# Kernel optimization log

Hardware: AMD Instinct MI355X
Metric: run time of the kernel (lower is better)

Reference implementation:

```python
import jax, jax.numpy as jnp
import numpy as np

N, M, BS = 32, 64, 512
ALPHA, BETA = 1.0, 1.0


def setup_inputs() -> dict:
    key = jax.random.key(0)
    k1, k2, k3, k4 = jax.random.split(key, 4)
    q = jax.random.normal(k1, (BS, N), jnp.float32)
    b = jax.random.normal(k2, (BS, M), jnp.float32)
    A0 = jax.random.normal(k3, (N, N), jnp.float32)
    P = A0 @ A0.T / N + jnp.eye(N, dtype=jnp.float32)  # SPD cost matrix
    H = jax.random.normal(k4, (M, N), jnp.float32) / jnp.sqrt(jnp.float32(N))
    return {"q": q, "b": b, "P": P, "H": H, "iters": 1000}


def reference(q, b, P, H, iters):
    m = H.shape[0]
    # Pinv-applied quantities via solve (matches torch.linalg.solve / pinv usage)
    Pinv_q = jnp.linalg.solve(P, q.T).T                 # (bs, n)
    D = H @ jnp.linalg.solve(P, H.T)                    # (m, m) = H P^-1 H^T
    # dummy preconditioner: scaled identity keeping the operator nonexpansive
    lam_max = jnp.linalg.eigvalsh(D)[-1]
    tD = (BETA / lam_max) * jnp.eye(m, dtype=q.dtype)   # (m, m)
    mu = ((H @ Pinv_q.T).T - b) @ tD.T                  # (bs, m)
    tDD = tD @ D
    I = jnp.eye(m, dtype=q.dtype)
    A = jnp.block([[tDD, tD],
                   [-2.0 * ALPHA * tDD + I, I - 2.0 * ALPHA * tD]])  # (2m, 2m)
    B = jnp.concatenate([mu, -2.0 * ALPHA * mu], axis=1)             # (bs, 2m)
    Hinv = jnp.linalg.pinv(H)                            # (n, m)
    X0 = jnp.zeros((q.shape[0], 2 * m), q.dtype)

    def step(X, _):
        X = X @ A.T + B
        X = X.at[:, m:].set(jax.nn.relu(X[:, m:]))       # in-place ReLU on dual half
        return X, X

    _, ys = jax.lax.scan(step, X0, None, length=iters)   # (iters, bs, 2m)
    Xs = jnp.concatenate([X0[None], ys], axis=0).transpose(1, 0, 2)  # (bs, iters+1, 2m)
    # primal_sols[k] = Hinv @ (X_k[m:] - b)
    primal_sols = jnp.einsum('nm,bkm->bkn', Hinv, Xs[:, :, m:] - b[:, None, :])
    return Xs, primal_sols
```

## Files before the change

### kernel.cpp

```cpp
#include <hip/hip_runtime.h>
#include <math.h>

#define BATCH 512
#define ITERS 1000

#define OFF_S    0
#define OFF_SD   16
#define OFF_PHT  (16 + 4096)
#define OFF_HINV (16 + 4096 + 2048)

__device__ __forceinline__ float rdlane(float v, int l) {
  return __int_as_float(__builtin_amdgcn_readlane(__float_as_int(v), l));
}

#define GJ32_REG(g)                                            \
  _Pragma("unroll")                                            \
  for (int k = 0; k < 32; ++k) {                               \
    float inv = 1.0f / rdlane(g[k], k);                        \
    g[k] *= inv;                                               \
    _Pragma("unroll")                                          \
    for (int i = 0; i < 32; ++i) {                             \
      if (i == k) continue;                                    \
      float f = rdlane(g[i], k);                               \
      g[i] = fmaf(-f, g[k], g[i]);                             \
    }                                                          \
  }

__global__ __launch_bounds__(64) void setup_kernel(const float* __restrict__ P,
                                                   const float* __restrict__ H,
                                                   float* __restrict__ ws) {
  __shared__ float Hl[64][36];
  const int lane = threadIdx.x;

  float hreg[32];
  {
    const float4* hp = (const float4*)(H + lane * 32);
    #pragma unroll
    for (int j4 = 0; j4 < 8; ++j4) {
      float4 t = hp[j4];
      hreg[4*j4+0] = t.x; hreg[4*j4+1] = t.y; hreg[4*j4+2] = t.z; hreg[4*j4+3] = t.w;
    }
  }

  if (blockIdx.x == 0) {
    float g[32];
    #pragma unroll
    for (int r = 0; r < 32; ++r) {
      float pv = P[r*32 + (lane & 31)];
      g[r] = (lane < 32) ? pv : (((lane - 32) == r) ? 1.0f : 0.0f);
    }
    GJ32_REG(g)

    float pht[32];
    #pragma unroll
    for (int r = 0; r < 32; ++r) {
      float a0 = 0.f, a1 = 0.f;
      #pragma unroll
      for (int j = 0; j < 32; j += 2) {
        a0 = fmaf(rdlane(g[r], 32 + j),     hreg[j],     a0);
        a1 = fmaf(rdlane(g[r], 32 + j + 1), hreg[j + 1], a1);
      }
      pht[r] = a0 + a1;
      ws[OFF_PHT + r*64 + lane] = pht[r];
    }

    float dcol[64];
    #pragma unroll
    for (int r = 0; r < 64; ++r) {
      float a0 = 0.f, a1 = 0.f;
      #pragma unroll
      for (int j = 0; j < 32; j += 2) {
        a0 = fmaf(rdlane(hreg[j],     r), pht[j],     a0);
        a1 = fmaf(rdlane(hreg[j + 1], r), pht[j + 1], a1);
      }
      dcol[r] = a0 + a1;
    }

    float ecol[64];
    #pragma unroll
    for (int r = 0; r < 64; ++r) {
      float a0 = 0.f, a1 = 0.f;
      #pragma unroll
      for (int c = 0; c < 64; c += 2) {
        a0 = fmaf(rdlane(dcol[r], c),     dcol[c],     a0);
        a1 = fmaf(rdlane(dcol[r], c + 1), dcol[c + 1], a1);
      }
      ecol[r] = a0 + a1;
    }

    float v = 1.0f + 0.017f * (float)lane;
    #pragma unroll 1
    for (int t = 0; t < 112; ++t) {
      float a0 = 0.f, a1 = 0.f, a2 = 0.f, a3 = 0.f;
      #pragma unroll
      for (int c = 0; c < 64; c += 4) {
        a0 = fmaf(ecol[c+0], rdlane(v, c+0), a0);
        a1 = fmaf(ecol[c+1], rdlane(v, c+1), a1);
        a2 = fmaf(ecol[c+2], rdlane(v, c+2), a2);
        a3 = fmaf(ecol[c+3], rdlane(v, c+3), a3);
      }
      v = (a0 + a1) + (a2 + a3);
      if ((t & 7) == 7) {
        float n2 = v * v;
        #pragma unroll
        for (int m = 1; m < 64; m <<= 1) n2 += __shfl_xor(n2, m);
        v *= 1.0f / sqrtf(n2);
      }
    }
    {
      float a0 = 0.f, a1 = 0.f, a2 = 0.f, a3 = 0.f;
      #pragma unroll
      for (int c = 0; c < 64; c += 4) {
        a0 = fmaf(dcol[c+0], rdlane(v, c+0), a0);
        a1 = fmaf(dcol[c+1], rdlane(v, c+1), a1);
        a2 = fmaf(dcol[c+2], rdlane(v, c+2), a2);
        a3 = fmaf(dcol[c+3], rdlane(v, c+3), a3);
      }
      float w = (a0 + a1) + (a2 + a3);
      float num = w * v, den = v * v;
      #pragma unroll
      for (int m = 1; m < 64; m <<= 1) {
        num += __shfl_xor(num, m);
        den += __shfl_xor(den, m);
      }
      float s = den / num;
      if (lane == 0) ws[OFF_S] = s;
      #pragma unroll
      for (int r = 0; r < 64; ++r) ws[OFF_SD + r*64 + lane] = s * dcol[r];
    }
  } else {
    #pragma unroll
    for (int j = 0; j < 32; ++j) Hl[lane][j] = hreg[j];
    __syncthreads();
    float htc[64];
    #pragma unroll
    for (int m = 0; m < 64; ++m) htc[m] = Hl[m][lane & 31];

    float gB[32];
    #pragma unroll
    for (int r = 0; r < 32; ++r) {
      float a0 = 0.f, a1 = 0.f;
      #pragma unroll
      for (int m = 0; m < 64; m += 2) {
        a0 = fmaf(rdlane(hreg[r], m),     htc[m],     a0);
        a1 = fmaf(rdlane(hreg[r], m + 1), htc[m + 1], a1);
      }
      float hth = a0 + a1;
      gB[r] = (lane < 32) ? hth : (((lane - 32) == r) ? 1.0f : 0.0f);
    }
    GJ32_REG(gB)
    #pragma unroll
    for (int r = 0; r < 32; ++r) {
      float a0 = 0.f, a1 = 0.f;
      #pragma unroll
      for (int j = 0; j < 32; j += 2) {
        a0 = fmaf(rdlane(gB[r], 32 + j),     hreg[j],     a0);
        a1 = fmaf(rdlane(gB[r], 32 + j + 1), hreg[j + 1], a1);
      }
      ws[OFF_HINV + r*64 + lane] = a0 + a1;
    }
  }
}

__global__ __launch_bounds__(64) void iter_kernel(const float* __restrict__ q,
                                                  const float* __restrict__ bmat,
                                                  const float* __restrict__ ws,
                                                  float* __restrict__ Xs) {
  const int row = blockIdx.x, lane = threadIdx.x;

  float sdr[64];
  {
    const float4* sp = (const float4*)(ws + OFF_SD + lane * 64);
    #pragma unroll
    for (int j4 = 0; j4 < 16; ++j4) {
      float4 t = sp[j4];
      sdr[4*j4+0] = t.x; sdr[4*j4+1] = t.y; sdr[4*j4+2] = t.z; sdr[4*j4+3] = t.w;
    }
  }
  const float s = ws[OFF_S];
  float acc = 0.f;
  {
    const float* qrow = q + row * 32;
    #pragma unroll
    for (int j = 0; j < 32; ++j) acc = fmaf(qrow[j], ws[OFF_PHT + j*64 + lane], acc);
  }
  const float mu = s * (acc - bmat[row * 64 + lane]);

  float x1 = 0.f, x2 = 0.f;
  float* Xp = Xs + (size_t)row * (ITERS + 1) * 128;
  Xp[lane] = 0.f;
  Xp[64 + lane] = 0.f;

  #pragma unroll 1
  for (int k = 1; k <= ITERS; ++k) {
    float a0 = 0.f, a1 = 0.f, a2 = 0.f, a3 = 0.f;
    #pragma unroll
    for (int j = 0; j < 64; j += 4) {
      a0 = fmaf(sdr[j+0], rdlane(x1, j+0), a0);
      a1 = fmaf(sdr[j+1], rdlane(x1, j+1), a1);
      a2 = fmaf(sdr[j+2], rdlane(x1, j+2), a2);
      a3 = fmaf(sdr[j+3], rdlane(x1, j+3), a3);
    }
    float x1n = ((a0 + a1) + (a2 + a3)) + fmaf(s, x2, mu);
    float x2n = fmaxf(x1 + x2 - 2.0f * x1n, 0.f);
    Xp += 128;
    Xp[lane] = x1n;
    Xp[64 + lane] = x2n;
    x1 = x1n; x2 = x2n;
  }
}

__global__ __launch_bounds__(512) void primal_kernel(const float* __restrict__ bmat,
                                                     const float* __restrict__ ws,
                                                     const float* __restrict__ Xs,
                                                     float* __restrict__ out2) {
  const int row = blockIdx.x;
  const int tid = threadIdx.x;
  const int wv = tid >> 6, lane = tid & 63;
  const int i = lane & 31, h = lane >> 5;
  __shared__ __align__(16) float tbuf[8][64];

  float hv[32];
  {
    const float4* hp = (const float4*)(ws + OFF_HINV + i * 64 + h * 32);
    #pragma unroll
    for (int j4 = 0; j4 < 8; ++j4) {
      float4 t = hp[j4];
      hv[4*j4+0] = t.x; hv[4*j4+1] = t.y; hv[4*j4+2] = t.z; hv[4*j4+3] = t.w;
    }
  }
  const float bl = bmat[row * 64 + lane];
  const float* Xb = Xs + (size_t)row * (ITERS + 1) * 128 + 64;
  float* ob = out2 + (size_t)row * (ITERS + 1) * 32;

  float tA = Xb[(size_t)wv * 128 + lane] - bl;
  float tB = (wv + 8 <= ITERS) ? Xb[(size_t)(wv + 8) * 128 + lane] - bl : 0.f;

  #pragma unroll 1
  for (int k = wv; k <= ITERS; k += 8) {
    const int kn = k + 16;
    float tC = (kn <= ITERS) ? Xb[(size_t)kn * 128 + lane] - bl : 0.f;
    tbuf[wv][lane] = tA;
    __builtin_amdgcn_wave_barrier();
    float a0 = 0.f, a1 = 0.f, a2 = 0.f, a3 = 0.f;
    const float4* tp = (const float4*)&tbuf[wv][h * 32];
    #pragma unroll
    for (int j4 = 0; j4 < 8; ++j4) {
      float4 t = tp[j4];
      a0 = fmaf(hv[4*j4+0], t.x, a0);
      a1 = fmaf(hv[4*j4+1], t.y, a1);
      a2 = fmaf(hv[4*j4+2], t.z, a2);
      a3 = fmaf(hv[4*j4+3], t.w, a3);
    }
    float p = (a0 + a1) + (a2 + a3);
    p += __shfl_xor(p, 32);
    if (h == 0) ob[(size_t)k * 32 + i] = p;
    __builtin_amdgcn_wave_barrier();
    tA = tB; tB = tC;
  }
}

extern "C" void kernel_launch(void* const* d_in, const int* in_sizes, int n_in,
                              void* d_out, int out_size, void* d_ws, size_t ws_size,
                              hipStream_t stream) {
  (void)in_sizes; (void)n_in; (void)out_size; (void)ws_size;
  const float* q = (const float*)d_in[0];
  const float* b = (const float*)d_in[1];
  const float* P = (const float*)d_in[2];
  const float* H = (const float*)d_in[3];
  float* ws = (float*)d_ws;
  float* Xs = (float*)d_out;
  float* out2 = Xs + (size_t)BATCH * (ITERS + 1) * 128;

  setup_kernel<<<2, 64, 0, stream>>>(P, H, ws);
  iter_kernel<<<BATCH, 64, 0, stream>>>(q, b, ws, Xs);
  primal_kernel<<<BATCH, 512, 0, stream>>>(b, ws, Xs, out2);
}
```

Baseline: 685.1 us.

## Fuse setup, iteration and primal projection into one kernel per batch row

Merges the three kernels into one. Each block redundantly recomputes the setup quantities (P inverse, H pseudo-inverse, the power-iteration eigenvalue and the scaled D) and then runs the recurrence. The primal projection for step k-1 is computed inside step k from a double-buffered LDS copy of the dual half, so the primal kernel no longer has to read Xs back from global memory and the extra launches and workspace traffic disappear. The cost is that every one of the 512 blocks repeats the serial setup work, about two 32x32 Gauss-Jordan eliminations plus 112 power iterations, before its loop can start.

```diff
diff --git a/kernel.cpp b/kernel.cpp
--- a/kernel.cpp
+++ b/kernel.cpp
@@ -4,13 +4,18 @@
 #define BATCH 512
 #define ITERS 1000
 
-#define OFF_S    0
-#define OFF_SD   16
-#define OFF_PHT  (16 + 4096)
-#define OFF_HINV (16 + 4096 + 2048)
+typedef float f32x2 __attribute__((ext_vector_type(2)));
+typedef float f32x4 __attribute__((ext_vector_type(4)));
 
 __device__ __forceinline__ float rdlane(float v, int l) {
   return __int_as_float(__builtin_amdgcn_readlane(__float_as_int(v), l));
+}
+__device__ __forceinline__ f32x2 fma2(f32x2 a, f32x2 b, f32x2 c) {
+#if __has_builtin(__builtin_elementwise_fma)
+  return __builtin_elementwise_fma(a, b, c);
+#else
+  f32x2 r; r.x = fmaf(a.x, b.x, c.x); r.y = fmaf(a.y, b.y, c.y); return r;
+#endif
 }
 
 #define GJ32_REG(g)                                            \
@@ -19,39 +24,88 @@
     float inv = 1.0f / rdlane(g[k], k);                        \
     g[k] *= inv;                                               \
     _Pragma("unroll")                                          \
-    for (int i = 0; i < 32; ++i) {                             \
-      if (i == k) continue;                                    \
-      float f = rdlane(g[i], k);                               \
-      g[i] = fmaf(-f, g[k], g[i]);                             \
+    for (int ii = 0; ii < 32; ++ii) {                          \
+      if (ii == k) continue;                                   \
+      float f = rdlane(g[ii], k);                              \
+      g[ii] = fmaf(-f, g[k], g[ii]);                           \
     }                                                          \
   }
 
-__global__ __launch_bounds__(64) void setup_kernel(const float* __restrict__ P,
-                                                   const float* __restrict__ H,
-                                                   float* __restrict__ ws) {
-  __shared__ float Hl[64][36];
-  const int lane = threadIdx.x;
+__global__ __launch_bounds__(64, 1)
+void fused_kernel(const float* __restrict__ q,
+                  const float* __restrict__ bmat,
+                  const float* __restrict__ P,
+                  const float* __restrict__ H,
+                  float* __restrict__ Xs,
+                  float* __restrict__ out2) {
+  __shared__ __align__(16) float lds[2112 + 128];
+  float* Hlp = lds;
+  float* HTp = lds;
+  float* xb  = lds + 2112;
+
+  const int row = blockIdx.x, lane = threadIdx.x;
+  const int i = lane & 31, h = lane >> 5;
+
+  const float bl = bmat[row * 64 + lane];
 
   float hreg[32];
   {
-    const float4* hp = (const float4*)(H + lane * 32);
+    const f32x4* hp = (const f32x4*)(H + lane * 32);
     #pragma unroll
     for (int j4 = 0; j4 < 8; ++j4) {
-      float4 t = hp[j4];
+      f32x4 t = hp[j4];
       hreg[4*j4+0] = t.x; hreg[4*j4+1] = t.y; hreg[4*j4+2] = t.z; hreg[4*j4+3] = t.w;
     }
-  }
-
-  if (blockIdx.x == 0) {
+    #pragma unroll
+    for (int j = 0; j < 32; ++j) Hlp[lane * 33 + j] = hreg[j];
+  }
+  __syncthreads();
+
+  f32x2 hv2[16];
+  {
+    float htc[64];
+    #pragma unroll
+    for (int m = 0; m < 64; ++m) htc[m] = Hlp[m * 33 + i];
+
+    float gB[32];
+    #pragma unroll
+    for (int r = 0; r < 32; ++r) {
+      float a0 = 0.f, a1 = 0.f;
+      #pragma unroll
+      for (int m = 0; m < 64; m += 2) {
+        a0 = fmaf(rdlane(hreg[r], m),     htc[m],     a0);
+        a1 = fmaf(rdlane(hreg[r], m + 1), htc[m + 1], a1);
+      }
+      float hth = a0 + a1;
+      gB[r] = (lane < 32) ? hth : (((lane - 32) == r) ? 1.0f : 0.0f);
+    }
+    GJ32_REG(gB)
+    __syncthreads();
+    #pragma unroll
+    for (int r = 0; r < 32; ++r) {
+      float a0 = 0.f, a1 = 0.f;
+      #pragma unroll
+      for (int c = 0; c < 32; c += 2) {
+        a0 = fmaf(rdlane(gB[r], 32 + c),     hreg[c],     a0);
+        a1 = fmaf(rdlane(gB[r], 32 + c + 1), hreg[c + 1], a1);
+      }
+      HTp[r * 66 + lane] = a0 + a1;
+    }
+    __syncthreads();
+    #pragma unroll
+    for (int t = 0; t < 16; ++t)
+      hv2[t] = *(const f32x2*)&HTp[i * 66 + 32 * h + 2 * t];
+  }
+
+  float pht[32], dcol[64], acc;
+  {
     float g[32];
     #pragma unroll
     for (int r = 0; r < 32; ++r) {
-      float pv = P[r*32 + (lane & 31)];
+      float pv = P[r * 32 + i];
       g[r] = (lane < 32) ? pv : (((lane - 32) == r) ? 1.0f : 0.0f);
     }
     GJ32_REG(g)
-
-    float pht[32];
     #pragma unroll
     for (int r = 0; r < 32; ++r) {
       float a0 = 0.f, a1 = 0.f;
@@ -61,21 +115,30 @@
         a1 = fmaf(rdlane(g[r], 32 + j + 1), hreg[j + 1], a1);
       }
       pht[r] = a0 + a1;
-      ws[OFF_PHT + r*64 + lane] = pht[r];
-    }
-
-    float dcol[64];
-    #pragma unroll
-    for (int r = 0; r < 64; ++r) {
-      float a0 = 0.f, a1 = 0.f;
-      #pragma unroll
-      for (int j = 0; j < 32; j += 2) {
-        a0 = fmaf(rdlane(hreg[j],     r), pht[j],     a0);
-        a1 = fmaf(rdlane(hreg[j + 1], r), pht[j + 1], a1);
-      }
-      dcol[r] = a0 + a1;
-    }
-
+    }
+  }
+  {
+    const float* qp = q + row * 32;
+    float a0 = 0.f, a1 = 0.f;
+    #pragma unroll
+    for (int r = 0; r < 32; r += 2) {
+      a0 = fmaf(qp[r],     pht[r],     a0);
+      a1 = fmaf(qp[r + 1], pht[r + 1], a1);
+    }
+    acc = a0 + a1;
+  }
+  #pragma unroll
+  for (int r = 0; r < 64; ++r) {
+    float a0 = 0.f, a1 = 0.f;
+    #pragma unroll
+    for (int j = 0; j < 32; j += 2) {
+      a0 = fmaf(rdlane(hreg[j],     r), pht[j],     a0);
+      a1 = fmaf(rdlane(hreg[j + 1], r), pht[j + 1], a1);
+    }
+    dcol[r] = a0 + a1;
+  }
+  float s;
+  {
     float ecol[64];
     #pragma unroll
     for (int r = 0; r < 64; ++r) {
@@ -87,7 +150,6 @@
       }
       ecol[r] = a0 + a1;
     }
-
     float v = 1.0f + 0.017f * (float)lane;
     #pragma unroll 1
     for (int t = 0; t < 112; ++t) {
@@ -107,172 +169,97 @@
         v *= 1.0f / sqrtf(n2);
       }
     }
-    {
-      float a0 = 0.f, a1 = 0.f, a2 = 0.f, a3 = 0.f;
-      #pragma unroll
-      for (int c = 0; c < 64; c += 4) {
-        a0 = fmaf(dcol[c+0], rdlane(v, c+0), a0);
-        a1 = fmaf(dcol[c+1], rdlane(v, c+1), a1);
-        a2 = fmaf(dcol[c+2], rdlane(v, c+2), a2);
-        a3 = fmaf(dcol[c+3], rdlane(v, c+3), a3);
-      }
-      float w = (a0 + a1) + (a2 + a3);
-      float num = w * v, den = v * v;
-      #pragma unroll
-      for (int m = 1; m < 64; m <<= 1) {
-        num += __shfl_xor(num, m);
-        den += __shfl_xor(den, m);
-      }
-      float s = den / num;
-      if (lane == 0) ws[OFF_S] = s;
-      #pragma unroll
-      for (int r = 0; r < 64; ++r) ws[OFF_SD + r*64 + lane] = s * dcol[r];
-    }
-  } else {
-    #pragma unroll
-    for (int j = 0; j < 32; ++j) Hl[lane][j] = hreg[j];
-    __syncthreads();
-    float htc[64];
-    #pragma unroll
-    for (int m = 0; m < 64; ++m) htc[m] = Hl[m][lane & 31];
-
-    float gB[32];
-    #pragma unroll
-    for (int r = 0; r < 32; ++r) {
-      float a0 = 0.f, a1 = 0.f;
-      #pragma unroll
-      for (int m = 0; m < 64; m += 2) {
-        a0 = fmaf(rdlane(hreg[r], m),     htc[m],     a0);
-        a1 = fmaf(rdlane(hreg[r], m + 1), htc[m + 1], a1);
-      }
-      float hth = a0 + a1;
-      gB[r] = (lane < 32) ? hth : (((lane - 32) == r) ? 1.0f : 0.0f);
-    }
-    GJ32_REG(gB)
-    #pragma unroll
-    for (int r = 0; r < 32; ++r) {
-      float a0 = 0.f, a1 = 0.f;
-      #pragma unroll
-      for (int j = 0; j < 32; j += 2) {
-        a0 = fmaf(rdlane(gB[r], 32 + j),     hreg[j],     a0);
-        a1 = fmaf(rdlane(gB[r], 32 + j + 1), hreg[j + 1], a1);
-      }
-      ws[OFF_HINV + r*64 + lane] = a0 + a1;
-    }
-  }
-}
-
-__global__ __launch_bounds__(64) void iter_kernel(const float* __restrict__ q,
-                                                  const float* __restrict__ bmat,
-                                                  const float* __restrict__ ws,
-                                                  float* __restrict__ Xs) {
-  const int row = blockIdx.x, lane = threadIdx.x;
-
-  float sdr[64];
-  {
-    const float4* sp = (const float4*)(ws + OFF_SD + lane * 64);
-    #pragma unroll
-    for (int j4 = 0; j4 < 16; ++j4) {
-      float4 t = sp[j4];
-      sdr[4*j4+0] = t.x; sdr[4*j4+1] = t.y; sdr[4*j4+2] = t.z; sdr[4*j4+3] = t.w;
-    }
-  }
-  const float s = ws[OFF_S];
-  float acc = 0.f;
-  {
-    const float* qrow = q + row * 32;
-    #pragma unroll
-    for (int j = 0; j < 32; ++j) acc = fmaf(qrow[j], ws[OFF_PHT + j*64 + lane], acc);
-  }
-  const float mu = s * (acc - bmat[row * 64 + lane]);
-
-  float x1 = 0.f, x2 = 0.f;
+    float a0 = 0.f, a1 = 0.f, a2 = 0.f, a3 = 0.f;
+    #pragma unroll
+    for (int c = 0; c < 64; c += 4) {
+      a0 = fmaf(dcol[c+0], rdlane(v, c+0), a0);
+      a1 = fmaf(dcol[c+1], rdlane(v, c+1), a1);
+      a2 = fmaf(dcol[c+2], rdlane(v, c+2), a2);
+      a3 = fmaf(dcol[c+3], rdlane(v, c+3), a3);
+    }
+    float w = (a0 + a1) + (a2 + a3);
+    float num = w * v, den = v * v;
+    #pragma unroll
+    for (int m = 1; m < 64; m <<= 1) {
+      num += __shfl_xor(num, m);
+      den += __shfl_xor(den, m);
+    }
+    s = den / num;
+  }
+  const float mu = s * (acc - bl);
+  #pragma unroll
+  for (int r = 0; r < 64; ++r) dcol[r] *= s;
+
   float* Xp = Xs + (size_t)row * (ITERS + 1) * 128;
+  float* ob = out2 + (size_t)row * (ITERS + 1) * 32;
   Xp[lane] = 0.f;
   Xp[64 + lane] = 0.f;
-
+  xb[lane] = -bl;
+
+  float x1 = 0.f, x2 = 0.f;
   #pragma unroll 1
   for (int k = 1; k <= ITERS; ++k) {
+    const f32x4* tp = (const f32x4*)(xb + ((k - 1) & 1) * 64 + h * 32);
+    f32x4 t0 = tp[0], t1 = tp[1], t2 = tp[2], t3 = tp[3];
+    f32x4 t4 = tp[4], t5 = tp[5], t6 = tp[6], t7 = tp[7];
+
     float a0 = 0.f, a1 = 0.f, a2 = 0.f, a3 = 0.f;
     #pragma unroll
     for (int j = 0; j < 64; j += 4) {
-      a0 = fmaf(sdr[j+0], rdlane(x1, j+0), a0);
-      a1 = fmaf(sdr[j+1], rdlane(x1, j+1), a1);
-      a2 = fmaf(sdr[j+2], rdlane(x1, j+2), a2);
-      a3 = fmaf(sdr[j+3], rdlane(x1, j+3), a3);
+      a0 = fmaf(dcol[j+0], rdlane(x1, j+0), a0);
+      a1 = fmaf(dcol[j+1], rdlane(x1, j+1), a1);
+      a2 = fmaf(dcol[j+2], rdlane(x1, j+2), a2);
+      a3 = fmaf(dcol[j+3], rdlane(x1, j+3), a3);
     }
     float x1n = ((a0 + a1) + (a2 + a3)) + fmaf(s, x2, mu);
-    float x2n = fmaxf(x1 + x2 - 2.0f * x1n, 0.f);
+    float x2n = fmaxf(fmaf(-2.0f, x1n, x1 + x2), 0.f);
     Xp += 128;
     Xp[lane] = x1n;
     Xp[64 + lane] = x2n;
+    xb[(k & 1) * 64 + lane] = x2n - bl;
+
+    f32x2 pa; pa.x = 0.f; pa.y = 0.f;
+    f32x2 pb = pa;
+    pa = fma2(hv2[0],  t0.xy, pa);  pb = fma2(hv2[1],  t0.zw, pb);
+    pa = fma2(hv2[2],  t1.xy, pa);  pb = fma2(hv2[3],  t1.zw, pb);
+    pa = fma2(hv2[4],  t2.xy, pa);  pb = fma2(hv2[5],  t2.zw, pb);
+    pa = fma2(hv2[6],  t3.xy, pa);  pb = fma2(hv2[7],  t3.zw, pb);
+    pa = fma2(hv2[8],  t4.xy, pa);  pb = fma2(hv2[9],  t4.zw, pb);
+    pa = fma2(hv2[10], t5.xy, pa);  pb = fma2(hv2[11], t5.zw, pb);
+    pa = fma2(hv2[12], t6.xy, pa);  pb = fma2(hv2[13], t6.zw, pb);
+    pa = fma2(hv2[14], t7.xy, pa);  pb = fma2(hv2[15], t7.zw, pb);
+    float p = (pa.x + pa.y) + (pb.x + pb.y);
+    p += __shfl_xor(p, 32);
+    if (h == 0) ob[(size_t)(k - 1) * 32 + i] = p;
+
     x1 = x1n; x2 = x2n;
   }
-}
-
-__global__ __launch_bounds__(512) void primal_kernel(const float* __restrict__ bmat,
-                                                     const float* __restrict__ ws,
-                                                     const float* __restrict__ Xs,
-                                                     float* __restrict__ out2) {
-  const int row = blockIdx.x;
-  const int tid = threadIdx.x;
-  const int wv = tid >> 6, lane = tid & 63;
-  const int i = lane & 31, h = lane >> 5;
-  __shared__ __align__(16) float tbuf[8][64];
-
-  float hv[32];
-  {
-    const float4* hp = (const float4*)(ws + OFF_HINV + i * 64 + h * 32);
-    #pragma unroll
-    for (int j4 = 0; j4 < 8; ++j4) {
-      float4 t = hp[j4];
-      hv[4*j4+0] = t.x; hv[4*j4+1] = t.y; hv[4*j4+2] = t.z; hv[4*j4+3] = t.w;
-    }
-  }
-  const float bl = bmat[row * 64 + lane];
-  const float* Xb = Xs + (size_t)row * (ITERS + 1) * 128 + 64;
-  float* ob = out2 + (size_t)row * (ITERS + 1) * 32;
-
-  float tA = Xb[(size_t)wv * 128 + lane] - bl;
-  float tB = (wv + 8 <= ITERS) ? Xb[(size_t)(wv + 8) * 128 + lane] - bl : 0.f;
-
-  #pragma unroll 1
-  for (int k = wv; k <= ITERS; k += 8) {
-    const int kn = k + 16;
-    float tC = (kn <= ITERS) ? Xb[(size_t)kn * 128 + lane] - bl : 0.f;
-    tbuf[wv][lane] = tA;
-    __builtin_amdgcn_wave_barrier();
-    float a0 = 0.f, a1 = 0.f, a2 = 0.f, a3 = 0.f;
-    const float4* tp = (const float4*)&tbuf[wv][h * 32];
-    #pragma unroll
-    for (int j4 = 0; j4 < 8; ++j4) {
-      float4 t = tp[j4];
-      a0 = fmaf(hv[4*j4+0], t.x, a0);
-      a1 = fmaf(hv[4*j4+1], t.y, a1);
-      a2 = fmaf(hv[4*j4+2], t.z, a2);
-      a3 = fmaf(hv[4*j4+3], t.w, a3);
-    }
-    float p = (a0 + a1) + (a2 + a3);
+  {
+    const f32x4* tp = (const f32x4*)(xb + (ITERS & 1) * 64 + h * 32);
+    f32x2 pa; pa.x = 0.f; pa.y = 0.f;
+    f32x2 pb = pa;
+    #pragma unroll
+    for (int r4 = 0; r4 < 8; ++r4) {
+      f32x4 t = tp[r4];
+      pa = fma2(hv2[2*r4],     t.xy, pa);
+      pb = fma2(hv2[2*r4 + 1], t.zw, pb);
+    }
+    float p = (pa.x + pa.y) + (pb.x + pb.y);
     p += __shfl_xor(p, 32);
-    if (h == 0) ob[(size_t)k * 32 + i] = p;
-    __builtin_amdgcn_wave_barrier();
-    tA = tB; tB = tC;
+    if (h == 0) ob[(size_t)ITERS * 32 + i] = p;
   }
 }
 
 extern "C" void kernel_launch(void* const* d_in, const int* in_sizes, int n_in,
                               void* d_out, int out_size, void* d_ws, size_t ws_size,
                               hipStream_t stream) {
-  (void)in_sizes; (void)n_in; (void)out_size; (void)ws_size;
+  (void)in_sizes; (void)n_in; (void)out_size; (void)d_ws; (void)ws_size;
   const float* q = (const float*)d_in[0];
   const float* b = (const float*)d_in[1];
   const float* P = (const float*)d_in[2];
   const float* H = (const float*)d_in[3];
-  float* ws = (float*)d_ws;
   float* Xs = (float*)d_out;
   float* out2 = Xs + (size_t)BATCH * (ITERS + 1) * 128;
 
-  setup_kernel<<<2, 64, 0, stream>>>(P, H, ws);
-  iter_kernel<<<BATCH, 64, 0, stream>>>(q, b, ws, Xs);
-  primal_kernel<<<BATCH, 512, 0, stream>>>(b, ws, Xs, out2);
-}
+  fused_kernel<<<BATCH, 64, 0, stream>>>(q, b, P, H, Xs, out2);
+}
```

Result: slower. 739.5 us (+7.9%).

## Recompute P-inverse, D and spectral scale redundantly per block inside iter kernel

Applied to the files above, without the earlier changes.

The serial setup work (Gauss-Jordan inverse of P, P^-1 H^T, D, and the 112-step power iteration for lambda_max) moves out of a single-block setup kernel into every iter_kernel block. Each block recomputes it redundantly so the iteration no longer waits on a serial setup launch and reads no workspace. The pseudo-inverse of H stays in its own small kernel. The cost is 512 copies of the setup arithmetic, with higher register pressure in iter_kernel before the main loop.

```diff
diff --git a/kernel.cpp b/kernel.cpp
--- a/kernel.cpp
+++ b/kernel.cpp
@@ -4,13 +4,18 @@
 #define BATCH 512
 #define ITERS 1000
 
-#define OFF_S    0
-#define OFF_SD   16
-#define OFF_PHT  (16 + 4096)
-#define OFF_HINV (16 + 4096 + 2048)
+typedef float f32x2 __attribute__((ext_vector_type(2)));
+typedef float f32x4 __attribute__((ext_vector_type(4)));
 
 __device__ __forceinline__ float rdlane(float v, int l) {
   return __int_as_float(__builtin_amdgcn_readlane(__float_as_int(v), l));
+}
+__device__ __forceinline__ f32x2 fma2(f32x2 a, f32x2 b, f32x2 c) {
+#if __has_builtin(__builtin_elementwise_fma)
+  return __builtin_elementwise_fma(a, b, c);
+#else
+  f32x2 r; r.x = fmaf(a.x, b.x, c.x); r.y = fmaf(a.y, b.y, c.y); return r;
+#endif
 }
 
 #define GJ32_REG(g)                                            \
@@ -19,52 +24,108 @@
     float inv = 1.0f / rdlane(g[k], k);                        \
     g[k] *= inv;                                               \
     _Pragma("unroll")                                          \
-    for (int i = 0; i < 32; ++i) {                             \
-      if (i == k) continue;                                    \
-      float f = rdlane(g[i], k);                               \
-      g[i] = fmaf(-f, g[k], g[i]);                             \
+    for (int ii = 0; ii < 32; ++ii) {                          \
+      if (ii == k) continue;                                   \
+      float f = rdlane(g[ii], k);                              \
+      g[ii] = fmaf(-f, g[k], g[ii]);                           \
     }                                                          \
   }
 
-__global__ __launch_bounds__(64) void setup_kernel(const float* __restrict__ P,
-                                                   const float* __restrict__ H,
-                                                   float* __restrict__ ws) {
-  __shared__ float Hl[64][36];
+__global__ __launch_bounds__(64) void hinv_kernel(const float* __restrict__ H,
+                                                  float* __restrict__ ws) {
+  __shared__ float hstage[64 * 34];
   const int lane = threadIdx.x;
-
+  const int l = lane & 31;
   float hreg[32];
   {
-    const float4* hp = (const float4*)(H + lane * 32);
-    #pragma unroll
-    for (int j4 = 0; j4 < 8; ++j4) {
-      float4 t = hp[j4];
+    const f32x4* hp = (const f32x4*)(H + lane * 32);
+    #pragma unroll
+    for (int j4 = 0; j4 < 8; ++j4) {
+      f32x4 t = hp[j4];
       hreg[4*j4+0] = t.x; hreg[4*j4+1] = t.y; hreg[4*j4+2] = t.z; hreg[4*j4+3] = t.w;
     }
   }
-
-  if (blockIdx.x == 0) {
-    float g[32];
-    #pragma unroll
-    for (int r = 0; r < 32; ++r) {
-      float pv = P[r*32 + (lane & 31)];
-      g[r] = (lane < 32) ? pv : (((lane - 32) == r) ? 1.0f : 0.0f);
-    }
-    GJ32_REG(g)
-
-    float pht[32];
-    #pragma unroll
-    for (int r = 0; r < 32; ++r) {
+  #pragma unroll
+  for (int j = 0; j < 32; ++j) hstage[lane * 34 + j] = hreg[j];
+  float htc[64];
+  #pragma unroll
+  for (int m = 0; m < 64; ++m) htc[m] = hstage[m * 34 + l];
+  float gB[32];
+  #pragma unroll
+  for (int r = 0; r < 32; ++r) {
+    float a0 = 0.f, a1 = 0.f;
+    #pragma unroll
+    for (int m = 0; m < 64; m += 2) {
+      a0 = fmaf(rdlane(hreg[r], m),     htc[m],     a0);
+      a1 = fmaf(rdlane(hreg[r], m + 1), htc[m + 1], a1);
+    }
+    float hth = a0 + a1;
+    gB[r] = (lane < 32) ? hth : (((lane - 32) == r) ? 1.0f : 0.0f);
+  }
+  GJ32_REG(gB)
+  #pragma unroll
+  for (int r = 0; r < 32; ++r) {
+    float a0 = 0.f, a1 = 0.f;
+    #pragma unroll
+    for (int c = 0; c < 32; c += 2) {
+      a0 = fmaf(rdlane(gB[r], 32 + c),     hreg[c],     a0);
+      a1 = fmaf(rdlane(gB[r], 32 + c + 1), hreg[c + 1], a1);
+    }
+    ws[r * 64 + lane] = a0 + a1;
+  }
+}
+
+__global__ __launch_bounds__(64) void iter_kernel(const float* __restrict__ q,
+                                                  const float* __restrict__ bmat,
+                                                  const float* __restrict__ P,
+                                                  const float* __restrict__ H,
+                                                  float* __restrict__ Xs) {
+  const int row = blockIdx.x, lane = threadIdx.x;
+  const int i = lane & 31;
+
+  float hreg[32];
+  {
+    const f32x4* hp = (const f32x4*)(H + lane * 32);
+    #pragma unroll
+    for (int j4 = 0; j4 < 8; ++j4) {
+      f32x4 t = hp[j4];
+      hreg[4*j4+0] = t.x; hreg[4*j4+1] = t.y; hreg[4*j4+2] = t.z; hreg[4*j4+3] = t.w;
+    }
+  }
+  const float bl = bmat[(size_t)row * 64 + lane];
+
+  float dcol[64], s, mu;
+  {
+    float pht[32], acc;
+    {
+      float g[32];
+      #pragma unroll
+      for (int r = 0; r < 32; ++r) {
+        float pv = P[r * 32 + i];
+        g[r] = (lane < 32) ? pv : (((lane - 32) == r) ? 1.0f : 0.0f);
+      }
+      GJ32_REG(g)
+      #pragma unroll
+      for (int r = 0; r < 32; ++r) {
+        float a0 = 0.f, a1 = 0.f;
+        #pragma unroll
+        for (int j = 0; j < 32; j += 2) {
+          a0 = fmaf(rdlane(g[r], 32 + j),     hreg[j],     a0);
+          a1 = fmaf(rdlane(g[r], 32 + j + 1), hreg[j + 1], a1);
+        }
+        pht[r] = a0 + a1;
+      }
+    }
+    {
+      const float* qp = q + (size_t)row * 32;
       float a0 = 0.f, a1 = 0.f;
       #pragma unroll
-      for (int j = 0; j < 32; j += 2) {
-        a0 = fmaf(rdlane(g[r], 32 + j),     hreg[j],     a0);
-        a1 = fmaf(rdlane(g[r], 32 + j + 1), hreg[j + 1], a1);
-      }
-      pht[r] = a0 + a1;
-      ws[OFF_PHT + r*64 + lane] = pht[r];
-    }
-
-    float dcol[64];
+      for (int r = 0; r < 32; r += 2) {
+        a0 = fmaf(qp[r],     pht[r],     a0);
+        a1 = fmaf(qp[r + 1], pht[r + 1], a1);
+      }
+      acc = a0 + a1;
+    }
     #pragma unroll
     for (int r = 0; r < 64; ++r) {
       float a0 = 0.f, a1 = 0.f;
@@ -75,39 +136,37 @@
       }
       dcol[r] = a0 + a1;
     }
-
-    float ecol[64];
-    #pragma unroll
-    for (int r = 0; r < 64; ++r) {
-      float a0 = 0.f, a1 = 0.f;
-      #pragma unroll
-      for (int c = 0; c < 64; c += 2) {
-        a0 = fmaf(rdlane(dcol[r], c),     dcol[c],     a0);
-        a1 = fmaf(rdlane(dcol[r], c + 1), dcol[c + 1], a1);
-      }
-      ecol[r] = a0 + a1;
-    }
-
-    float v = 1.0f + 0.017f * (float)lane;
-    #pragma unroll 1
-    for (int t = 0; t < 112; ++t) {
-      float a0 = 0.f, a1 = 0.f, a2 = 0.f, a3 = 0.f;
-      #pragma unroll
-      for (int c = 0; c < 64; c += 4) {
-        a0 = fmaf(ecol[c+0], rdlane(v, c+0), a0);
-        a1 = fmaf(ecol[c+1], rdlane(v, c+1), a1);
-        a2 = fmaf(ecol[c+2], rdlane(v, c+2), a2);
-        a3 = fmaf(ecol[c+3], rdlane(v, c+3), a3);
-      }
-      v = (a0 + a1) + (a2 + a3);
-      if ((t & 7) == 7) {
-        float n2 = v * v;
+    {
+      float ecol[64];
+      #pragma unroll
+      for (int r = 0; r < 64; ++r) {
+        float a0 = 0.f, a1 = 0.f;
         #pragma unroll
-        for (int m = 1; m < 64; m <<= 1) n2 += __shfl_xor(n2, m);
-        v *= 1.0f / sqrtf(n2);
-      }
-    }
-    {
+        for (int c = 0; c < 64; c += 2) {
+          a0 = fmaf(rdlane(dcol[r], c),     dcol[c],     a0);
+          a1 = fmaf(rdlane(dcol[r], c + 1), dcol[c + 1], a1);
+        }
+        ecol[r] = a0 + a1;
+      }
+      float v = 1.0f + 0.017f * (float)lane;
+      #pragma unroll 1
+      for (int t = 0; t < 112; ++t) {
+        float a0 = 0.f, a1 = 0.f, a2 = 0.f, a3 = 0.f;
+        #pragma unroll
+        for (int c = 0; c < 64; c += 4) {
+          a0 = fmaf(ecol[c+0], rdlane(v, c+0), a0);
+          a1 = fmaf(ecol[c+1], rdlane(v, c+1), a1);
+          a2 = fmaf(ecol[c+2], rdlane(v, c+2), a2);
+          a3 = fmaf(ecol[c+3], rdlane(v, c+3), a3);
+        }
+        v = (a0 + a1) + (a2 + a3);
+        if ((t & 7) == 7) {
+          float n2 = v * v;
+          #pragma unroll
+          for (int m = 1; m < 64; m <<= 1) n2 += __shfl_xor(n2, m);
+          v *= 1.0f / sqrtf(n2);
+        }
+      }
       float a0 = 0.f, a1 = 0.f, a2 = 0.f, a3 = 0.f;
       #pragma unroll
       for (int c = 0; c < 64; c += 4) {
@@ -123,68 +182,12 @@
         num += __shfl_xor(num, m);
         den += __shfl_xor(den, m);
       }
-      float s = den / num;
-      if (lane == 0) ws[OFF_S] = s;
-      #pragma unroll
-      for (int r = 0; r < 64; ++r) ws[OFF_SD + r*64 + lane] = s * dcol[r];
-    }
-  } else {
-    #pragma unroll
-    for (int j = 0; j < 32; ++j) Hl[lane][j] = hreg[j];
-    __syncthreads();
-    float htc[64];
-    #pragma unroll
-    for (int m = 0; m < 64; ++m) htc[m] = Hl[m][lane & 31];
-
-    float gB[32];
-    #pragma unroll
-    for (int r = 0; r < 32; ++r) {
-      float a0 = 0.f, a1 = 0.f;
-      #pragma unroll
-      for (int m = 0; m < 64; m += 2) {
-        a0 = fmaf(rdlane(hreg[r], m),     htc[m],     a0);
-        a1 = fmaf(rdlane(hreg[r], m + 1), htc[m + 1], a1);
-      }
-      float hth = a0 + a1;
-      gB[r] = (lane < 32) ? hth : (((lane - 32) == r) ? 1.0f : 0.0f);
-    }
-    GJ32_REG(gB)
-    #pragma unroll
-    for (int r = 0; r < 32; ++r) {
-      float a0 = 0.f, a1 = 0.f;
-      #pragma unroll
-      for (int j = 0; j < 32; j += 2) {
-        a0 = fmaf(rdlane(gB[r], 32 + j),     hreg[j],     a0);
-        a1 = fmaf(rdlane(gB[r], 32 + j + 1), hreg[j + 1], a1);
-      }
-      ws[OFF_HINV + r*64 + lane] = a0 + a1;
-    }
-  }
-}
-
-__global__ __launch_bounds__(64) void iter_kernel(const float* __restrict__ q,
-                                                  const float* __restrict__ bmat,
-                                                  const float* __restrict__ ws,
-                                                  float* __restrict__ Xs) {
-  const int row = blockIdx.x, lane = threadIdx.x;
-
-  float sdr[64];
-  {
-    const float4* sp = (const float4*)(ws + OFF_SD + lane * 64);
-    #pragma unroll
-    for (int j4 = 0; j4 < 16; ++j4) {
-      float4 t = sp[j4];
-      sdr[4*j4+0] = t.x; sdr[4*j4+1] = t.y; sdr[4*j4+2] = t.z; sdr[4*j4+3] = t.w;
-    }
-  }
-  const float s = ws[OFF_S];
-  float acc = 0.f;
-  {
-    const float* qrow = q + row * 32;
-    #pragma unroll
-    for (int j = 0; j < 32; ++j) acc = fmaf(qrow[j], ws[OFF_PHT + j*64 + lane], acc);
-  }
-  const float mu = s * (acc - bmat[row * 64 + lane]);
+      s = den / num;
+    }
+    mu = s * (acc - bl);
+    #pragma unroll
+    for (int r = 0; r < 64; ++r) dcol[r] *= s;
+  }
 
   float x1 = 0.f, x2 = 0.f;
   float* Xp = Xs + (size_t)row * (ITERS + 1) * 128;
@@ -196,13 +199,13 @@
     float a0 = 0.f, a1 = 0.f, a2 = 0.f, a3 = 0.f;
     #pragma unroll
     for (int j = 0; j < 64; j += 4) {
-      a0 = fmaf(sdr[j+0], rdlane(x1, j+0), a0);
-      a1 = fmaf(sdr[j+1], rdlane(x1, j+1), a1);
-      a2 = fmaf(sdr[j+2], rdlane(x1, j+2), a2);
-      a3 = fmaf(sdr[j+3], rdlane(x1, j+3), a3);
+      a0 = fmaf(dcol[j+0], rdlane(x1, j+0), a0);
+      a1 = fmaf(dcol[j+1], rdlane(x1, j+1), a1);
+      a2 = fmaf(dcol[j+2], rdlane(x1, j+2), a2);
+      a3 = fmaf(dcol[j+3], rdlane(x1, j+3), a3);
     }
     float x1n = ((a0 + a1) + (a2 + a3)) + fmaf(s, x2, mu);
-    float x2n = fmaxf(x1 + x2 - 2.0f * x1n, 0.f);
+    float x2n = fmaxf(fmaf(-2.0f, x1n, x1 + x2), 0.f);
     Xp += 128;
     Xp[lane] = x1n;
     Xp[64 + lane] = x2n;
@@ -222,14 +225,14 @@
 
   float hv[32];
   {
-    const float4* hp = (const float4*)(ws + OFF_HINV + i * 64 + h * 32);
-    #pragma unroll
-    for (int j4 = 0; j4 < 8; ++j4) {
-      float4 t = hp[j4];
+    const f32x4* hp = (const f32x4*)(ws + i * 64 + h * 32);
+    #pragma unroll
+    for (int j4 = 0; j4 < 8; ++j4) {
+      f32x4 t = hp[j4];
       hv[4*j4+0] = t.x; hv[4*j4+1] = t.y; hv[4*j4+2] = t.z; hv[4*j4+3] = t.w;
     }
   }
-  const float bl = bmat[row * 64 + lane];
+  const float bl = bmat[(size_t)row * 64 + lane];
   const float* Xb = Xs + (size_t)row * (ITERS + 1) * 128 + 64;
   float* ob = out2 + (size_t)row * (ITERS + 1) * 32;
 
@@ -243,10 +246,10 @@
     tbuf[wv][lane] = tA;
     __builtin_amdgcn_wave_barrier();
     float a0 = 0.f, a1 = 0.f, a2 = 0.f, a3 = 0.f;
-    const float4* tp = (const float4*)&tbuf[wv][h * 32];
-    #pragma unroll
-    for (int j4 = 0; j4 < 8; ++j4) {
-      float4 t = tp[j4];
+    const f32x4* tp = (const f32x4*)&tbuf[wv][h * 32];
+    #pragma unroll
+    for (int j4 = 0; j4 < 8; ++j4) {
+      f32x4 t = tp[j4];
       a0 = fmaf(hv[4*j4+0], t.x, a0);
       a1 = fmaf(hv[4*j4+1], t.y, a1);
       a2 = fmaf(hv[4*j4+2], t.z, a2);
@@ -272,7 +275,7 @@
   float* Xs = (float*)d_out;
   float* out2 = Xs + (size_t)BATCH * (ITERS + 1) * 128;
 
-  setup_kernel<<<2, 64, 0, stream>>>(P, H, ws);
-  iter_kernel<<<BATCH, 64, 0, stream>>>(q, b, ws, Xs);
+  hinv_kernel<<<1, 64, 0, stream>>>(H, ws);
+  iter_kernel<<<BATCH, 64, 0, stream>>>(q, b, P, H, Xs);
   primal_kernel<<<BATCH, 512, 0, stream>>>(b, ws, Xs, out2);
 }
```

Measured after the change: 718.2 us. 4.8% more time.
